# Performance work log

Measured on AMD Instinct MI355X. Metric: run time of the kernel, lower is better.

## Reference

```python
import jax, jax.numpy as jnp
import numpy as np

N = 50000     # nodes
E = 600000    # directed edges (avg degree 12)
F_IN = 128    # num_features
H = 128       # hidden_units
C = 16        # num_classes
G = 500       # graphs in batch


def setup_inputs() -> dict:
    key = jax.random.key(0)
    ks = jax.random.split(key, 6)
    x = jax.random.normal(ks[0], (N, F_IN), jnp.float32)
    edge_src = jax.random.randint(ks[1], (E,), 0, N, jnp.int32)
    edge_dst = jax.random.randint(ks[2], (E,), 0, N, jnp.int32)
    batch = jnp.sort(jax.random.randint(ks[3], (N,), 0, G, jnp.int32))
    W1 = jax.random.normal(ks[4], (F_IN, H), jnp.float32) / np.float32(np.sqrt(F_IN))
    b1 = jnp.zeros((H,), jnp.float32)
    W2 = jax.random.normal(ks[5], (H, C), jnp.float32) / np.float32(np.sqrt(H))
    b2 = jnp.zeros((C,), jnp.float32)
    return {"x": x, "W1": W1, "b1": b1, "W2": W2, "b2": b2,
            "edge_src": edge_src, "edge_dst": edge_dst, "batch": batch}


def _gcn_conv(x, W, b, src, dst, norm):
    # linear transform then normalized scatter-add aggregation (PyG GCNConv)
    h = x @ W                                   # [N, out]
    msg = h[src] * norm[:, None]                # [E+N, out]
    return jax.ops.segment_sum(msg, dst, num_segments=N) + b


def reference(x, W1, b1, W2, b2, edge_src, edge_dst, batch):
    # add self-loops
    loops = jnp.arange(N, dtype=edge_src.dtype)
    src = jnp.concatenate([edge_src, loops])
    dst = jnp.concatenate([edge_dst, loops])
    # symmetric normalization D^-1/2 A D^-1/2 (in-degree at targets)
    deg = jax.ops.segment_sum(jnp.ones_like(dst, jnp.float32), dst, num_segments=N)
    dis = jax.lax.rsqrt(deg)  # deg >= 1 because of self-loops
    norm = dis[src] * dis[dst]

    h = jax.nn.relu(_gcn_conv(x, W1, b1, src, dst, norm))
    h = _gcn_conv(h, W2, b2, src, dst, norm)

    # scatter_mean pooling over graphs
    counts = jax.ops.segment_sum(jnp.ones((N,), jnp.float32), batch, num_segments=G)
    pooled = jax.ops.segment_sum(h, batch, num_segments=G) / jnp.maximum(counts, 1.0)[:, None]
    return jax.nn.log_softmax(pooled, axis=1)
```

## Files before the change

kernel.cpp:

```cpp
#include <hip/hip_runtime.h>
#include <hip/hip_bf16.h>


#define NN 50000
#define EE 600000
#define FIN 128
#define HH 128
#define CC 16
#define GG 500
#define ETOT (EE + NN)
#define SBLK 196
#define WTS 140
#define CBLK ((EE + 255) / 256)
#define A1CAP 1024
#define A2CAP 2048

typedef unsigned short ushort_t;
typedef unsigned int uint_t;

typedef __attribute__((ext_vector_type(8))) short bf16x8;
typedef __attribute__((ext_vector_type(4))) ushort_t u16x4;
typedef __attribute__((ext_vector_type(4))) float f32x4;
typedef __attribute__((ext_vector_type(2))) float f32x2;

__device__ inline ushort_t f2bf(float f) {
    uint_t u = __float_as_uint(f);
    u = (u + 0x7FFFu + ((u >> 16) & 1u)) >> 16;
    return (ushort_t)u;
}
__device__ inline float bf2f(ushort_t b) {
    return __uint_as_float(((uint_t)b) << 16);
}
__device__ inline ushort_t f2h(float f) {
    _Float16 h = (_Float16)f; ushort_t u; __builtin_memcpy(&u, &h, 2); return u;
}
__device__ inline float h2f(ushort_t u) {
    _Float16 h; __builtin_memcpy(&h, &u, 2); return (float)h;
}

__global__ void init_kernel(int* cnt, float* pooled) {
    int i = blockIdx.x * blockDim.x + threadIdx.x;
    if (i < NN) cnt[i] = 0;
    if (i < GG * CC) pooled[i] = 0.0f;
}

__global__ __launch_bounds__(256) void cg1_kernel(const int* __restrict__ edge_dst,
                                                  int* __restrict__ cnt,
                                                  int* __restrict__ seq,
                                                  const float* __restrict__ x,
                                                  const float* __restrict__ W1,
                                                  unsigned char* __restrict__ hb8) {
    __shared__ ushort_t xs[64 * 136];
    __shared__ ushort_t wt[128 * WTS];
    if (blockIdx.x < CBLK) {
        int idx = blockIdx.x * 256 + threadIdx.x;
        if (idx < EE) seq[idx] = atomicAdd(&cnt[edge_dst[idx]], 1);
        return;
    }
    int t = threadIdx.x;
    int row0 = (blockIdx.x - CBLK) * 64;
    for (int i = 0; i < 8; i++) {
        int slot = t + i * 256;
        int r = slot >> 5, k4 = slot & 31;
        int gr = row0 + r;
        float4 v = (gr < NN) ? ((const float4*)x)[gr * 32 + k4]
                             : make_float4(0.f, 0.f, 0.f, 0.f);
        u16x4 bv = { f2bf(v.x), f2bf(v.y), f2bf(v.z), f2bf(v.w) };
        *(u16x4*)(&xs[r * 136 + k4 * 4]) = bv;
    }
    for (int i = 0; i < 16; i++) {
        int idx = t + i * 256;
        int c = idx & 127, k4 = idx >> 7;
        u16x4 bv = { f2bf(W1[(4 * k4 + 0) * HH + c]),
                     f2bf(W1[(4 * k4 + 1) * HH + c]),
                     f2bf(W1[(4 * k4 + 2) * HH + c]),
                     f2bf(W1[(4 * k4 + 3) * HH + c]) };
        *(u16x4*)(&wt[c * WTS + k4 * 4]) = bv;
    }
    __syncthreads();

    int wave = t >> 6, lane = t & 63;
    int m = lane & 15, quad = lane >> 4;
    f32x4 acc[8];
    for (int ct = 0; ct < 8; ct++) acc[ct] = (f32x4)(0.0f);
    for (int ko = 0; ko < 4; ko++) {
        bf16x8 a = *(const bf16x8*)(&xs[(16 * wave + m) * 136 + ko * 32 + quad * 8]);
        for (int ct = 0; ct < 8; ct++) {
            bf16x8 b = *(const bf16x8*)(&wt[(ct * 16 + m) * WTS + ko * 32 + quad * 8]);
            acc[ct] = __builtin_amdgcn_mfma_f32_16x16x32_bf16(a, b, acc[ct], 0, 0, 0);
        }
    }
    for (int ct = 0; ct < 8; ct++) {
        int gcol = ct * 16 + m;
        for (int r = 0; r < 4; r++) {
            int grow = row0 + wave * 16 + quad * 4 + r;
            if (grow < NN) {
                int p = __builtin_amdgcn_cvt_pk_fp8_f32(acc[ct][r], 0.0f, 0, false);
                hb8[(size_t)grow * HH + gcol] = (unsigned char)(p & 0xFF);
            }
        }
    }
}

__device__ inline int block_excl_scan(int v, int t, int* total) {
    __shared__ int wsum[4];
    int lane = t & 63, wv = t >> 6;
    int inc = v;
    for (int off = 1; off < 64; off <<= 1) {
        int n = __shfl_up(inc, off);
        if (lane >= off) inc += n;
    }
    if (lane == 63) wsum[wv] = inc;
    __syncthreads();
    int off_w = 0;
    for (int w = 0; w < wv; w++) off_w += wsum[w];
    *total = wsum[0] + wsum[1] + wsum[2] + wsum[3];
    return off_w + inc - v;
}

__global__ __launch_bounds__(256) void scanA_kernel(const int* __restrict__ cnt,
                                                    int* __restrict__ rowptr,
                                                    float* __restrict__ dis,
                                                    int* __restrict__ bsum,
                                                    const int* __restrict__ batch,
                                                    int* __restrict__ gstart) {
    int t = threadIdx.x;
    int i = blockIdx.x * 256 + t;
    int d = 0;
    if (i < NN) {
        d = cnt[i] + 1;
        dis[i] = rsqrtf((float)d);
        int b = batch[i];
        int bp = (i == 0) ? -1 : batch[i - 1];
        for (int g = bp + 1; g <= b; ++g) gstart[g] = i;
        if (i == NN - 1) {
            for (int g = b + 1; g <= GG; ++g) gstart[g] = NN;
        }
    }
    int total;
    int excl = block_excl_scan(d, t, &total);
    if (i < NN) rowptr[i] = excl;
    if (t == 0) bsum[blockIdx.x] = total;
}

__global__ __launch_bounds__(256) void scanBC_kernel(int* __restrict__ rowptr,
                                                     const int* __restrict__ bsum) {
    __shared__ int sb[256];
    int t = threadIdx.x;
    int v = (t < SBLK) ? bsum[t] : 0;
    int total;
    int ex = block_excl_scan(v, t, &total);
    sb[t] = ex;
    __syncthreads();
    int myoff = sb[blockIdx.x];
    int i = blockIdx.x * 256 + t;
    if (i < NN) rowptr[i] += myoff;
    if (blockIdx.x == 0 && t == 0) rowptr[NN] = ETOT;
}

__global__ void fill_kernel(const int* __restrict__ edge_src,
                            const int* __restrict__ edge_dst,
                            const float* __restrict__ dis,
                            const int* __restrict__ rowptr,
                            const int* __restrict__ seq,
                            uint_t* __restrict__ csr) {
    int idx = blockIdx.x * blockDim.x + threadIdx.x;
    if (idx < EE) {
        int s = edge_src[idx], d = edge_dst[idx];
        csr[rowptr[d] + seq[idx]] = (uint_t)s | ((uint_t)f2h(dis[s]) << 16);
    } else if (idx < ETOT) {
        int n = idx - EE;
        csr[rowptr[n + 1] - 1] = (uint_t)n | ((uint_t)f2h(dis[n]) << 16);
    }
}

__global__ __launch_bounds__(256, 4) void agg1f_kernel(const unsigned char* __restrict__ hb8,
                                                       const int* __restrict__ rowptr,
                                                       const uint_t* __restrict__ csr,
                                                       const float* __restrict__ dis,
                                                       const float* __restrict__ b1,
                                                       const float* __restrict__ W2,
                                                       ushort_t* __restrict__ h2b) {
    __shared__ uint_t w2s[8 * 132];
    __shared__ uint_t ecsr[A1CAP];
    int t = threadIdx.x;
    int node0 = blockIdx.x * 4;
    int wave = t >> 6, lane = t & 63;
    int node = node0 + wave;
    int slot = lane >> 3, sub = lane & 7;
    int wbeg = rowptr[node0];
    int wcap = rowptr[node0 + 4];
    int e0 = rowptr[node], e1 = rowptr[node + 1];
    float dn = dis[node];
    {
        const float2* W2v = (const float2*)W2;
        for (int i = t; i < HH * 8; i += 256) {
            int k = i >> 3, sl = i & 7;
            float2 wv = W2v[i];
            w2s[(k >> 4) * 132 + (k & 15) * 8 + sl] =
                (uint_t)f2bf(wv.x) | ((uint_t)f2bf(wv.y) << 16);
        }
    }
    int wlen = min(wcap - wbeg, A1CAP);
    for (int i = t; i < wlen; i += 256) ecsr[i] = csr[wbeg + i];
    __syncthreads();
    int wend = wbeg + wlen;

    float acc[16];
    for (int j = 0; j < 16; j++) acc[j] = 0.0f;
    for (int e = e0 + slot; e < e1; e += 16) {
        uint_t ent0;
        if (e < wend) ent0 = ecsr[e - wbeg]; else ent0 = csr[e];
        bool has2 = (e + 8) < e1;
        uint_t ent1 = ent0;
        if (has2) {
            if (e + 8 < wend) ent1 = ecsr[e + 8 - wbeg]; else ent1 = csr[e + 8];
        }
        uint4 hv0 = *(const uint4*)(hb8 + (size_t)(ent0 & 0xFFFFu) * HH + sub * 16);
        uint4 hv1 = has2 ? *(const uint4*)(hb8 + (size_t)(ent1 & 0xFFFFu) * HH + sub * 16)
                         : make_uint4(0, 0, 0, 0);
        float w0 = h2f((ushort_t)(ent0 >> 16));
        uint_t words0[4] = { hv0.x, hv0.y, hv0.z, hv0.w };
        for (int q = 0; q < 4; q++) {
            f32x2 lo = __builtin_amdgcn_cvt_pk_f32_fp8(words0[q], false);
            f32x2 hi = __builtin_amdgcn_cvt_pk_f32_fp8(words0[q], true);
            acc[q * 4 + 0] += w0 * lo[0];
            acc[q * 4 + 1] += w0 * lo[1];
            acc[q * 4 + 2] += w0 * hi[0];
            acc[q * 4 + 3] += w0 * hi[1];
        }
        if (has2) {
            float w1 = h2f((ushort_t)(ent1 >> 16));
            uint_t words1[4] = { hv1.x, hv1.y, hv1.z, hv1.w };
            for (int q = 0; q < 4; q++) {
                f32x2 lo = __builtin_amdgcn_cvt_pk_f32_fp8(words1[q], false);
                f32x2 hi = __builtin_amdgcn_cvt_pk_f32_fp8(words1[q], true);
                acc[q * 4 + 0] += w1 * lo[0];
                acc[q * 4 + 1] += w1 * lo[1];
                acc[q * 4 + 2] += w1 * hi[0];
                acc[q * 4 + 3] += w1 * hi[1];
            }
        }
    }
    for (int j = 0; j < 16; j++) {
        acc[j] += __shfl_xor(acc[j], 8);
        acc[j] += __shfl_xor(acc[j], 16);
        acc[j] += __shfl_xor(acc[j], 32);
    }
    const float4* b1v = (const float4*)(b1 + sub * 16);
    float4 bb[4] = { b1v[0], b1v[1], b1v[2], b1v[3] };
    const float* bbf = (const float*)bb;
    float p0 = 0.0f, p1 = 0.0f;
    int wbase = sub * 132 + slot;
    for (int j = 0; j < 16; j++) {
        float h = fmaxf(dn * acc[j] + bbf[j], 0.0f);
        uint_t w = w2s[wbase + j * 8];
        p0 += h * __uint_as_float(w << 16);
        p1 += h * __uint_as_float(w & 0xFFFF0000u);
    }
    p0 += __shfl_xor(p0, 1); p0 += __shfl_xor(p0, 2); p0 += __shfl_xor(p0, 4);
    p1 += __shfl_xor(p1, 1); p1 += __shfl_xor(p1, 2); p1 += __shfl_xor(p1, 4);
    if (sub == 0) {
        uint_t pk = (uint_t)f2bf(p0) | ((uint_t)f2bf(p1) << 16);
        *(uint_t*)(h2b + (size_t)node * CC + 2 * slot) = pk;
    }
}

__global__ __launch_bounds__(1024) void agg2pool_kernel(const ushort_t* __restrict__ h2b,
                                                        const int* __restrict__ rowptr,
                                                        const uint_t* __restrict__ csr,
                                                        const float* __restrict__ dis,
                                                        const float* __restrict__ b2,
                                                        const int* __restrict__ batch,
                                                        float* __restrict__ pooled) {
    __shared__ float vals[16][16];
    __shared__ int gid[16];
    __shared__ uint_t ecsr[A2CAP];
    int wave = threadIdx.x >> 6, lane = threadIdx.x & 63;
    int node0 = blockIdx.x * 16;
    int node = node0 + wave;
    int slot = lane >> 3, sub = lane & 7;
    int wbeg = rowptr[node0];
    int wcap = rowptr[node0 + 16];
    int e0 = rowptr[node], e1 = rowptr[node + 1];
    float dn = dis[node];
    int   bg = batch[node];
    float b20 = b2[2 * sub], b21 = b2[2 * sub + 1];
    int wlen = min(wcap - wbeg, A2CAP);
    for (int i = threadIdx.x; i < wlen; i += 1024) ecsr[i] = csr[wbeg + i];
    __syncthreads();
    int wend = wbeg + wlen;

    float a0 = 0.0f, a1 = 0.0f;
    for (int e = e0 + slot; e < e1; e += 16) {
        uint_t ent0;
        if (e < wend) ent0 = ecsr[e - wbeg]; else ent0 = csr[e];
        bool has2 = (e + 8) < e1;
        uint_t ent1 = ent0;
        if (has2) {
            if (e + 8 < wend) ent1 = ecsr[e + 8 - wbeg]; else ent1 = csr[e + 8];
        }
        uint_t p0 = *(const uint_t*)(h2b + (size_t)(ent0 & 0xFFFFu) * CC + sub * 2);
        uint_t p1 = has2 ? *(const uint_t*)(h2b + (size_t)(ent1 & 0xFFFFu) * CC + sub * 2) : 0;
        float w0 = h2f((ushort_t)(ent0 >> 16));
        a0 += w0 * bf2f((ushort_t)(p0 & 0xFFFFu));
        a1 += w0 * bf2f((ushort_t)(p0 >> 16));
        if (has2) {
            float w1 = h2f((ushort_t)(ent1 >> 16));
            a0 += w1 * bf2f((ushort_t)(p1 & 0xFFFFu));
            a1 += w1 * bf2f((ushort_t)(p1 >> 16));
        }
    }
    a0 += __shfl_xor(a0, 8); a0 += __shfl_xor(a0, 16); a0 += __shfl_xor(a0, 32);
    a1 += __shfl_xor(a1, 8); a1 += __shfl_xor(a1, 16); a1 += __shfl_xor(a1, 32);
    if (slot == 0) {
        vals[wave][2 * sub]     = a0 * dn + b20;
        vals[wave][2 * sub + 1] = a1 * dn + b21;
        if (sub == 0) gid[wave] = bg;
    }
    __syncthreads();
    if (threadIdx.x < 16) {
        int c = threadIdx.x;
        float run = 0.0f;
        for (int i = 0; i < 16; i++) {
            run += vals[i][c];
            if (i == 15 || gid[i + 1] != gid[i]) {
                atomicAdd(&pooled[gid[i] * CC + c], run);
                run = 0.0f;
            }
        }
    }
}

__global__ void lsm_kernel(const float* __restrict__ pooled,
                           const int* __restrict__ gstart,
                           float* __restrict__ out) {
    int idx = blockIdx.x * blockDim.x + threadIdx.x;
    int g = idx >> 4, c = idx & 15;
    if (g >= GG) return;
    float cnt = (float)(gstart[g + 1] - gstart[g]);
    float v = pooled[g * CC + c] / fmaxf(cnt, 1.0f);
    float m = v;
    for (int off = 8; off >= 1; off >>= 1) m = fmaxf(m, __shfl_xor(m, off, 16));
    float s = expf(v - m);
    for (int off = 8; off >= 1; off >>= 1) s += __shfl_xor(s, off, 16);
    out[g * CC + c] = v - m - logf(s);
}

extern "C" void kernel_launch(void* const* d_in, const int* in_sizes, int n_in,
                              void* d_out, int out_size, void* d_ws, size_t ws_size,
                              hipStream_t stream) {
    const float* x  = (const float*)d_in[0];
    const float* W1 = (const float*)d_in[1];
    const float* b1 = (const float*)d_in[2];
    const float* W2 = (const float*)d_in[3];
    const float* b2 = (const float*)d_in[4];
    const int* edge_src = (const int*)d_in[5];
    const int* edge_dst = (const int*)d_in[6];
    const int* batch    = (const int*)d_in[7];
    float* out = (float*)d_out;

    char* ws = (char*)d_ws;
    size_t off = 0;
    auto alloc = [&](size_t bytes) {
        void* p = ws + off;
        off += (bytes + 255) & ~size_t(255);
        return p;
    };
    int*   cnt     = (int*)  alloc(NN * 4);
    float* dis     = (float*)alloc(NN * 4);
    int*   rowptr  = (int*)  alloc((NN + 1) * 4);
    int*   seq     = (int*)  alloc(EE * 4);
    int*   bsum    = (int*)  alloc(SBLK * 4);
    uint_t* csr    = (uint_t*)alloc((size_t)ETOT * 4);
    unsigned char* hb8 = (unsigned char*)alloc((size_t)NN * HH);
    ushort_t* h2b  = (ushort_t*)alloc((size_t)NN * CC * 2);
    float* pooled  = (float*)alloc(GG * CC * 4);
    int*   gstart  = (int*)  alloc((GG + 1) * 4);

    const int B = 256;
    init_kernel<<<(NN + B - 1) / B, B, 0, stream>>>(cnt, pooled);
    cg1_kernel<<<CBLK + (NN + 63) / 64, B, 0, stream>>>(edge_dst, cnt, seq, x, W1, hb8);
    scanA_kernel<<<SBLK, B, 0, stream>>>(cnt, rowptr, dis, bsum, batch, gstart);
    scanBC_kernel<<<SBLK, B, 0, stream>>>(rowptr, bsum);
    fill_kernel<<<(ETOT + B - 1) / B, B, 0, stream>>>(edge_src, edge_dst, dis,
                                                      rowptr, seq, csr);
    agg1f_kernel<<<NN / 4, B, 0, stream>>>(hb8, rowptr, csr, dis, b1, W2, h2b);
    agg2pool_kernel<<<NN / 16, 1024, 0, stream>>>(h2b, rowptr, csr, dis, b2, batch, pooled);
    lsm_kernel<<<(GG * CC + B - 1) / B, B, 0, stream>>>(pooled, gstart, out);
}
```

Before: 196.4 us.

## Remap layer-1 aggregation to one wave per node with two features per lane

The layer-1 aggregation loop changes from 8 edge slots × 8 feature chunks of 16 bytes to every lane walking all edges of its node, each loading a 2-byte fp8 pair for its own 2 features. This removes the 48 cross-lane shuffles per node and the large per-lane accumulator array, at the cost of a serial edge loop with narrow 2-byte gathers instead of 16-byte ones. The ReLU'd hidden vector is staged in shared memory as bf16 so the existing W2 projection layout can still be used. A fast path skips the global-CSR fallback check when the block's edges fit the LDS cache.

```diff
diff --git a/kernel.cpp b/kernel.cpp
--- a/kernel.cpp
+++ b/kernel.cpp
@@ -183,6 +183,7 @@
                                                        ushort_t* __restrict__ h2b) {
     __shared__ uint_t w2s[8 * 132];
     __shared__ uint_t ecsr[A1CAP];
+    __shared__ uint_t h1s[4 * 64];
     int t = threadIdx.x;
     int node0 = blockIdx.x * 4;
     int wave = t >> 6, lane = t & 63;
@@ -192,6 +193,7 @@
     int wcap = rowptr[node0 + 4];
     int e0 = rowptr[node], e1 = rowptr[node + 1];
     float dn = dis[node];
+    float2 b1p = ((const float2*)b1)[lane];
     {
         const float2* W2v = (const float2*)W2;
         for (int i = t; i < HH * 8; i += 256) {
@@ -206,57 +208,43 @@
     __syncthreads();
     int wend = wbeg + wlen;
 
-    float acc[16];
-    for (int j = 0; j < 16; j++) acc[j] = 0.0f;
-    for (int e = e0 + slot; e < e1; e += 16) {
-        uint_t ent0;
-        if (e < wend) ent0 = ecsr[e - wbeg]; else ent0 = csr[e];
-        bool has2 = (e + 8) < e1;
-        uint_t ent1 = ent0;
-        if (has2) {
-            if (e + 8 < wend) ent1 = ecsr[e + 8 - wbeg]; else ent1 = csr[e + 8];
-        }
-        uint4 hv0 = *(const uint4*)(hb8 + (size_t)(ent0 & 0xFFFFu) * HH + sub * 16);
-        uint4 hv1 = has2 ? *(const uint4*)(hb8 + (size_t)(ent1 & 0xFFFFu) * HH + sub * 16)
-                         : make_uint4(0, 0, 0, 0);
-        float w0 = h2f((ushort_t)(ent0 >> 16));
-        uint_t words0[4] = { hv0.x, hv0.y, hv0.z, hv0.w };
-        for (int q = 0; q < 4; q++) {
-            f32x2 lo = __builtin_amdgcn_cvt_pk_f32_fp8(words0[q], false);
-            f32x2 hi = __builtin_amdgcn_cvt_pk_f32_fp8(words0[q], true);
-            acc[q * 4 + 0] += w0 * lo[0];
-            acc[q * 4 + 1] += w0 * lo[1];
-            acc[q * 4 + 2] += w0 * hi[0];
-            acc[q * 4 + 3] += w0 * hi[1];
-        }
-        if (has2) {
-            float w1 = h2f((ushort_t)(ent1 >> 16));
-            uint_t words1[4] = { hv1.x, hv1.y, hv1.z, hv1.w };
-            for (int q = 0; q < 4; q++) {
-                f32x2 lo = __builtin_amdgcn_cvt_pk_f32_fp8(words1[q], false);
-                f32x2 hi = __builtin_amdgcn_cvt_pk_f32_fp8(words1[q], true);
-                acc[q * 4 + 0] += w1 * lo[0];
-                acc[q * 4 + 1] += w1 * lo[1];
-                acc[q * 4 + 2] += w1 * hi[0];
-                acc[q * 4 + 3] += w1 * hi[1];
-            }
-        }
-    }
-    for (int j = 0; j < 16; j++) {
-        acc[j] += __shfl_xor(acc[j], 8);
-        acc[j] += __shfl_xor(acc[j], 16);
-        acc[j] += __shfl_xor(acc[j], 32);
-    }
-    const float4* b1v = (const float4*)(b1 + sub * 16);
-    float4 bb[4] = { b1v[0], b1v[1], b1v[2], b1v[3] };
-    const float* bbf = (const float*)bb;
+    f32x2 acc = { 0.0f, 0.0f };
+    if (wcap - wbeg <= A1CAP) {
+        for (int e = e0; e < e1; ++e) {
+            uint_t ent = ecsr[e - wbeg];
+            float ws = h2f((ushort_t)(ent >> 16));
+            uint_t pair = *(const ushort_t*)(hb8 + (size_t)(ent & 0xFFFFu) * HH + 2 * lane);
+            f32x2 v = __builtin_amdgcn_cvt_pk_f32_fp8(pair, false);
+            f32x2 wv = { ws, ws };
+            acc += wv * v;
+        }
+    } else {
+        for (int e = e0; e < e1; ++e) {
+            uint_t ent = (e < wend) ? ecsr[e - wbeg] : csr[e];
+            float ws = h2f((ushort_t)(ent >> 16));
+            uint_t pair = *(const ushort_t*)(hb8 + (size_t)(ent & 0xFFFFu) * HH + 2 * lane);
+            f32x2 v = __builtin_amdgcn_cvt_pk_f32_fp8(pair, false);
+            f32x2 wv = { ws, ws };
+            acc += wv * v;
+        }
+    }
+    float a0 = fmaxf(dn * acc[0] + b1p.x, 0.0f);
+    float a1 = fmaxf(dn * acc[1] + b1p.y, 0.0f);
+    h1s[wave * 64 + lane] = (uint_t)f2bf(a0) | ((uint_t)f2bf(a1) << 16);
+
     float p0 = 0.0f, p1 = 0.0f;
     int wbase = sub * 132 + slot;
-    for (int j = 0; j < 16; j++) {
-        float h = fmaxf(dn * acc[j] + bbf[j], 0.0f);
-        uint_t w = w2s[wbase + j * 8];
-        p0 += h * __uint_as_float(w << 16);
-        p1 += h * __uint_as_float(w & 0xFFFF0000u);
+    int hbase = wave * 64 + sub * 8;
+    for (int jj = 0; jj < 8; ++jj) {
+        uint_t hp = h1s[hbase + jj];
+        float he = bf2f((ushort_t)(hp & 0xFFFFu));
+        float ho = bf2f((ushort_t)(hp >> 16));
+        uint_t we = w2s[wbase + (2 * jj) * 8];
+        uint_t wo = w2s[wbase + (2 * jj + 1) * 8];
+        p0 += he * __uint_as_float(we << 16);
+        p1 += he * __uint_as_float(we & 0xFFFF0000u);
+        p0 += ho * __uint_as_float(wo << 16);
+        p1 += ho * __uint_as_float(wo & 0xFFFF0000u);
     }
     p0 += __shfl_xor(p0, 1); p0 += __shfl_xor(p0, 2); p0 += __shfl_xor(p0, 4);
     p1 += __shfl_xor(p1, 1); p1 += __shfl_xor(p1, 2); p1 += __shfl_xor(p1, 4);
```

Result: slower. 207.7 us (+5.8%).
